# Optimization experiments

Measured on AMD Instinct MI355X. Metric: run time of the kernel, lower is better.

The kernel has to match this reference:

```python
import jax, jax.numpy as jnp
import numpy as np

B, N = 32, 512
IN, HID, HEADS, OUT = 128, 32, 4, 128
NEG_SLOPE = 0.2


def _ln(x, g, b, eps=1e-5):
    mu = x.mean(-1, keepdims=True)
    var = ((x - mu) ** 2).mean(-1, keepdims=True)
    return (x - mu) * jax.lax.rsqrt(var + eps) * g + b


def _gat(x, adj_mask, W, a_src, a_dst, average):
    # x: [B,N,F], adj_mask: [B,1,N,N] bool, W: [F,H,D], a_*: [H,D]
    h = jnp.einsum('bnf,fhd->bnhd', x, W)                      # [B,N,H,D]
    e_src = jnp.einsum('bnhd,hd->bhn', h, a_src)               # [B,H,N]
    e_dst = jnp.einsum('bnhd,hd->bhn', h, a_dst)
    e = jax.nn.leaky_relu(e_src[:, :, :, None] + e_dst[:, :, None, :], NEG_SLOPE)  # [B,H,N,N]
    e = jnp.where(adj_mask, e, jnp.asarray(-1e9, e.dtype))
    att = jax.nn.softmax(e, axis=-1)                           # masked softmax over neighbors
    out = jnp.einsum('bhnm,bmhd->bnhd', att, h)                # aggregate neighbor features
    if average:
        return out.mean(axis=2)                                # [B,N,D]
    return out.reshape(out.shape[0], out.shape[1], -1)         # concat heads [B,N,H*D]


def setup_inputs() -> dict:
    key = jax.random.key(0)
    ks = jax.random.split(key, 16)
    def nrm(k, shape, scale=0.05):
        return jax.random.normal(k, shape, dtype=jnp.float32) * scale
    return {
        'x': jax.random.normal(ks[0], (B, N, IN), dtype=jnp.float32),
        'graph': jax.random.randint(ks[1], (B, N, N), 0, 2, dtype=jnp.int32),
        'W0': nrm(ks[2], (IN, HEADS, HID)),
        'a_src0': nrm(ks[3], (HEADS, HID)),
        'a_dst0': nrm(ks[4], (HEADS, HID)),
        'W1': nrm(ks[5], (HEADS * HID, 1, OUT)),
        'a_src1': nrm(ks[6], (1, OUT)),
        'a_dst1': nrm(ks[7], (1, OUT)),
        'ln1_g': jnp.ones((IN + OUT,), jnp.float32), 'ln1_b': jnp.zeros((IN + OUT,), jnp.float32),
        'lin_W': nrm(ks[8], (IN + OUT, OUT)), 'lin_b': jnp.zeros((OUT,), jnp.float32),
        'me_W0': nrm(ks[9], (OUT, OUT)), 'me_b0': jnp.zeros((OUT,), jnp.float32),
        'me_W1': nrm(ks[10], (OUT, OUT)), 'me_b1': jnp.zeros((OUT,), jnp.float32),
        'ln2_g': jnp.ones((OUT,), jnp.float32), 'ln2_b': jnp.zeros((OUT,), jnp.float32),
        'oh_W': nrm(ks[11], (OUT, OUT)), 'oh_b': jnp.zeros((OUT,), jnp.float32),
        'ln3_g': jnp.ones((OUT,), jnp.float32), 'ln3_b': jnp.zeros((OUT,), jnp.float32),
    }


def reference(x, graph, W0, a_src0, a_dst0, W1, a_src1, a_dst1,
              ln1_g, ln1_b, lin_W, lin_b, me_W0, me_b0, me_W1, me_b1,
              ln2_g, ln2_b, oh_W, oh_b, ln3_g, ln3_b):
    eye = jnp.eye(N, dtype=bool)
    adj_mask = ((graph > 0) | eye)[:, None, :, :]              # self-loops, [B,1,N,N]
    m = _gat(x, adj_mask, W0, a_src0, a_dst0, average=False)   # [B,N,HEADS*HID]
    m = jax.nn.elu(m)
    m = _gat(m, adj_mask, W1, a_src1, a_dst1, average=True)    # [B,N,OUT]
    m = _ln(jnp.concatenate([x, m], axis=-1), ln1_g, ln1_b)    # ln1
    m = m @ lin_W + lin_b                                      # linear
    enc = jax.nn.gelu(m @ me_W0 + me_b0, approximate=False) @ me_W1 + me_b1
    out = _ln(m + enc, ln2_g, ln2_b)                           # ln2(residual)
    out = jax.nn.gelu(out @ oh_W + oh_b, approximate=False)
    out = _ln(out, ln3_g, ln3_b)                               # LN inside output_head
    return out
```

## Files before the change

### kernel.cpp

```cpp
#include <hip/hip_runtime.h>
#include <cmath>


typedef unsigned short ushort_t;
typedef __attribute__((ext_vector_type(8))) short short8;
typedef __attribute__((ext_vector_type(4))) float f32x4;

__device__ __forceinline__ float gelu_f(float v) {
    return 0.5f * v * (1.0f + erff(v * 0.70710678118654752f));
}
__device__ __forceinline__ ushort_t f2bf(float x) {
    union { float f; unsigned u; } v; v.f = x;
    return (ushort_t)((v.u + 0x7FFFu + ((v.u >> 16) & 1u)) >> 16);
}
__device__ __forceinline__ ushort_t f2bf_t(float x) {
    union { float f; unsigned u; } v; v.f = x;
    return (ushort_t)(v.u >> 16);
}

__global__ __launch_bounds__(256) void prep_wt(const float* __restrict__ lin_W,
        const float* __restrict__ me_W0, const float* __restrict__ me_W1,
        const float* __restrict__ oh_W, const float* __restrict__ W0,
        const float* __restrict__ W1, ushort_t* __restrict__ WT) {
    int i = blockIdx.x * 256 + threadIdx.x;
    if (i < 32768)       { int c = i >> 8, k = i & 255;                   WT[i] = f2bf(lin_W[k * 128 + c]); }
    else if (i < 49152)  { int j = i - 32768;  int c = j >> 7, k = j & 127; WT[i] = f2bf(me_W0[k * 128 + c]); }
    else if (i < 65536)  { int j = i - 49152;  int c = j >> 7, k = j & 127; WT[i] = f2bf(me_W1[k * 128 + c]); }
    else if (i < 81920)  { int j = i - 65536;  int c = j >> 7, k = j & 127; WT[i] = f2bf(oh_W[k * 128 + c]); }
    else if (i < 98304)  { int j = i - 81920;  int c = j >> 7, k = j & 127; WT[i] = f2bf(W0[k * 128 + c]); }
    else if (i < 114688) { int j = i - 98304;  int c = j >> 7, k = j & 127; WT[i] = f2bf(W1[k * 128 + c]); }
}

__global__ __launch_bounds__(256) void gemm_mfma0(const float* __restrict__ X,
        const ushort_t* __restrict__ WTr, ushort_t* __restrict__ Ht,
        const float* __restrict__ a_s, const float* __restrict__ a_d,
        float* __restrict__ es, float* __restrict__ ed) {
    __shared__ __align__(16) ushort_t abuf[16 * 128];
    __shared__ __align__(16) ushort_t tb[128 * 24];
    __shared__ float2 ered[8 * 16];
    const int tid = threadIdx.x;
    const int row0 = blockIdx.x * 16;
    const int b = row0 >> 9, m0 = row0 & 511;
    const int w = tid >> 6, lane = tid & 63;
    const int quad = lane >> 4, lid = lane & 15;
    {
        int r = tid >> 4, g = tid & 15;
        const float4* src = (const float4*)(X + (row0 + r) * 128 + g * 8);
        float4 a = src[0], bb = src[1];
        short8 p;
        p[0] = (short)f2bf(a.x);  p[1] = (short)f2bf(a.y);
        p[2] = (short)f2bf(a.z);  p[3] = (short)f2bf(a.w);
        p[4] = (short)f2bf(bb.x); p[5] = (short)f2bf(bb.y);
        p[6] = (short)f2bf(bb.z); p[7] = (short)f2bf(bb.w);
        *(short8*)&abuf[r * 128 + ((g ^ (r & 7)) * 8)] = p;
    }
    __syncthreads();
    short8 af[4];
#pragma unroll
    for (int kc = 0; kc < 4; kc++)
        af[kc] = *(const short8*)&abuf[lid * 128 + (((kc * 4 + quad) ^ (lid & 7)) * 8)];
    f32x4 C[2];
#pragma unroll
    for (int i = 0; i < 2; i++) {
        int ct = w + 4 * i;
        const ushort_t* bp = WTr + (ct * 16 + lid) * 128 + quad * 8;
        C[i] = (f32x4){0.f, 0.f, 0.f, 0.f};
#pragma unroll
        for (int kc = 0; kc < 4; kc++) {
            short8 bf = *(const short8*)&bp[kc * 32];
            C[i] = __builtin_amdgcn_mfma_f32_16x16x32_bf16(af[kc], bf, C[i], 0, 0, 0);
        }
    }
#pragma unroll
    for (int i = 0; i < 2; i++) {
        int ct = w + 4 * i, col = ct * 16 + lid;
        float as_c = a_s[col], ad_c = a_d[col];
        float s0[4], d0[4];
#pragma unroll
        for (int r = 0; r < 4; r++) { s0[r] = C[i][r] * as_c; d0[r] = C[i][r] * ad_c; }
#pragma unroll
        for (int st = 1; st <= 8; st <<= 1)
#pragma unroll
            for (int r = 0; r < 4; r++) {
                s0[r] += __shfl_xor(s0[r], st);
                d0[r] += __shfl_xor(d0[r], st);
            }
        if (lid == 0) {
#pragma unroll
            for (int r = 0; r < 4; r++)
                ered[ct * 16 + quad * 4 + r] = make_float2(s0[r], d0[r]);
        }
#pragma unroll
        for (int r = 0; r < 4; r++)
            tb[col * 24 + quad * 4 + r] = f2bf(C[i][r]);
    }
    __syncthreads();
    if (tid < 64) {
        int row = tid & 15, h = tid >> 4;
        float2 pa = ered[(2 * h) * 16 + row], pb = ered[(2 * h + 1) * 16 + row];
        es[(b * 4 + h) * 512 + m0 + row] = pa.x + pb.x;
        ed[(b * 4 + h) * 512 + m0 + row] = pa.y + pb.y;
    }
    {
        int c = tid >> 1, half = tid & 1;
        *(short8*)&Ht[b * 65536 + c * 512 + m0 + half * 8] = *(const short8*)&tb[c * 24 + half * 8];
    }
}

__global__ __launch_bounds__(256) void gat0_gemm(const ushort_t* __restrict__ Ht0,
        const float* __restrict__ es0, const float* __restrict__ ed0,
        const int* __restrict__ graph, const ushort_t* __restrict__ W1T,
        const float* __restrict__ a_s, const float* __restrict__ a_d,
        ushort_t* __restrict__ Ht1, float* __restrict__ es1, float* __restrict__ ed1) {
    __shared__ __align__(16) char smem[33024];
    ushort_t* hsb  = (ushort_t*)smem;
    ushort_t* ps   = (ushort_t*)(smem + 16384);
    float*    eds  = (float*)(smem + 24576);
    float*    ess  = (float*)(smem + 32768);
    ushort_t* abuf = (ushort_t*)(smem + 16384);
    ushort_t* tb   = (ushort_t*)(smem + 24576);
    float2*   ered = (float2*)(smem + 30720);
    const int tid = threadIdx.x;
    const int b = blockIdx.y, n0 = blockIdx.x * 16;
    const int lane = tid & 63, wv = tid >> 6;
    const int quad = lane >> 4, lid = lane & 15;
    const int pn = tid >> 4, pg = (tid >> 1) & 7, ph = tid & 1;
    for (int i = tid; i < 2048; i += 256) eds[i] = ed0[b * 2048 + i];
    if (tid < 64) ess[tid] = es0[b * 2048 + (tid >> 4) * 512 + n0 + (tid & 15)];
    const short8 onesf = {0x3F80, 0x3F80, 0x3F80, 0x3F80, 0x3F80, 0x3F80, 0x3F80, 0x3F80};
    f32x4 acc[2], dsf;
    acc[0] = (f32x4){0.f, 0.f, 0.f, 0.f};
    acc[1] = (f32x4){0.f, 0.f, 0.f, 0.f};
    dsf = (f32x4){0.f, 0.f, 0.f, 0.f};
    for (int mc = 0; mc < 512; mc += 64) {
        __syncthreads();
        {
            const ushort_t* src = Ht0 + b * 65536 + mc;
            for (int u = tid; u < 1024; u += 256) {
                int c = u >> 3, g = u & 7;
                *(short8*)&hsb[c * 64 + ((g ^ (c & 7)) * 8)] = *(const short8*)&src[c * 512 + g * 8];
            }
        }
        {
            int ng = n0 + pn, mbase = mc + pg * 8;
            const int* grow = graph + (b * 512 + ng) * 512 + mbase;
            int4 ga = *(const int4*)grow;
            int4 gb = *(const int4*)(grow + 4);
            int gv[8] = {ga.x, ga.y, ga.z, ga.w, gb.x, gb.y, gb.z, gb.w};
            bool keep[8];
#pragma unroll
            for (int j = 0; j < 8; j++)
                keep[j] = (gv[j] > 0) | ((mbase + j) == ng);
#pragma unroll
            for (int hi = 0; hi < 2; hi++) {
                int hh = ph * 2 + hi;
                float es_v = ess[hh * 16 + pn];
                float4 e0v = *(const float4*)&eds[hh * 512 + mbase];
                float4 e1v = *(const float4*)&eds[hh * 512 + mbase + 4];
                float ev[8] = {e0v.x, e0v.y, e0v.z, e0v.w, e1v.x, e1v.y, e1v.z, e1v.w};
                short8 pk;
#pragma unroll
                for (int j = 0; j < 8; j++) {
                    float e = es_v + ev[j];
                    e = fmaxf(e, 0.2f * e);
                    e = keep[j] ? e : -1e30f;
                    pk[j] = (short)f2bf_t(__expf(e));
                }
                int prow = hh * 16 + pn;
                *(short8*)&ps[prow * 64 + ((pg ^ (prow & 7)) * 8)] = pk;
            }
        }
        __syncthreads();
#pragma unroll
        for (int kc = 0; kc < 2; kc++) {
            const int gsw = ((kc * 4 + quad) ^ (lid & 7)) * 8;
            short8 a = *(const short8*)&ps[(wv * 16 + lid) * 64 + gsw];
            short8 b0f = *(const short8*)&hsb[(wv * 32 + lid) * 64 + gsw];
            short8 b1f = *(const short8*)&hsb[(wv * 32 + 16 + lid) * 64 + gsw];
            acc[0] = __builtin_amdgcn_mfma_f32_16x16x32_bf16(a, b0f, acc[0], 0, 0, 0);
            acc[1] = __builtin_amdgcn_mfma_f32_16x16x32_bf16(a, b1f, acc[1], 0, 0, 0);
            dsf = __builtin_amdgcn_mfma_f32_16x16x32_bf16(a, onesf, dsf, 0, 0, 0);
        }
    }
    __syncthreads();
#pragma unroll
    for (int reg = 0; reg < 4; reg++) {
        float inv = 1.0f / dsf[reg];
        int rw = quad * 4 + reg;
#pragma unroll
        for (int ch = 0; ch < 2; ch++) {
            float v = acc[ch][reg] * inv;
            v = v > 0.f ? v : expm1f(v);
            int col = wv * 32 + ch * 16 + lid;
            abuf[rw * 128 + (((col >> 3) ^ (rw & 7)) * 8) + (col & 7)] = f2bf(v);
        }
    }
    __syncthreads();
    short8 af[4];
#pragma unroll
    for (int kc = 0; kc < 4; kc++)
        af[kc] = *(const short8*)&abuf[lid * 128 + (((kc * 4 + quad) ^ (lid & 7)) * 8)];
    f32x4 C[2];
#pragma unroll
    for (int i = 0; i < 2; i++) {
        int ct = wv + 4 * i;
        const ushort_t* bp = W1T + (ct * 16 + lid) * 128 + quad * 8;
        C[i] = (f32x4){0.f, 0.f, 0.f, 0.f};
#pragma unroll
        for (int kc = 0; kc < 4; kc++) {
            short8 bf = *(const short8*)&bp[kc * 32];
            C[i] = __builtin_amdgcn_mfma_f32_16x16x32_bf16(af[kc], bf, C[i], 0, 0, 0);
        }
    }
#pragma unroll
    for (int i = 0; i < 2; i++) {
        int ct = wv + 4 * i, col = ct * 16 + lid;
        float as_c = a_s[col], ad_c = a_d[col];
        float s0[4], d0[4];
#pragma unroll
        for (int r = 0; r < 4; r++) { s0[r] = C[i][r] * as_c; d0[r] = C[i][r] * ad_c; }
#pragma unroll
        for (int st = 1; st <= 8; st <<= 1)
#pragma unroll
            for (int r = 0; r < 4; r++) {
                s0[r] += __shfl_xor(s0[r], st);
                d0[r] += __shfl_xor(d0[r], st);
            }
        if (lid == 0) {
#pragma unroll
            for (int r = 0; r < 4; r++)
                ered[ct * 16 + quad * 4 + r] = make_float2(s0[r], d0[r]);
        }
#pragma unroll
        for (int r = 0; r < 4; r++)
            tb[col * 24 + quad * 4 + r] = f2bf(C[i][r]);
    }
    __syncthreads();
    if (tid < 16) {
        float S = 0.f, D = 0.f;
#pragma unroll
        for (int ct = 0; ct < 8; ct++) { float2 p = ered[ct * 16 + tid]; S += p.x; D += p.y; }
        es1[b * 512 + n0 + tid] = S;
        ed1[b * 512 + n0 + tid] = D;
    }
    {
        int c = tid >> 1, half = tid & 1;
        *(short8*)&Ht1[b * 65536 + c * 512 + n0 + half * 8] = *(const short8*)&tb[c * 24 + half * 8];
    }
}

__global__ __launch_bounds__(256) void gat1_head(const ushort_t* __restrict__ Ht,
        const float* __restrict__ es1, const float* __restrict__ ed1,
        const int* __restrict__ graph, const float* __restrict__ x,
        const float* __restrict__ g1, const float* __restrict__ b1,
        const ushort_t* __restrict__ linT, const float* __restrict__ LB,
        const ushort_t* __restrict__ meT0, const float* __restrict__ B0,
        const ushort_t* __restrict__ meT1, const float* __restrict__ B1,
        const float* __restrict__ g2, const float* __restrict__ b2,
        const ushort_t* __restrict__ ohT, const float* __restrict__ ob,
        const float* __restrict__ g3, const float* __restrict__ b3,
        float* __restrict__ out) {
    __shared__ __align__(16) char smem[25472];
    ushort_t* hsb  = (ushort_t*)smem;
    ushort_t* ps   = (ushort_t*)(smem + 16384);
    float*    eds  = (float*)(smem + 18432);
    float*    ess  = (float*)(smem + 20480);
    ushort_t* ybuf = (ushort_t*)smem;
    ushort_t* abuf = (ushort_t*)(smem + 8192);
    ushort_t* tbuf = (ushort_t*)(smem + 12288);
    float*    gbuf = (float*)(smem + 16384);
    float2*   red  = (float2*)(smem + 24832);
    float2*   mvs  = (float2*)(smem + 25344);
    const int tid = threadIdx.x;
    const int b = blockIdx.y, n0 = blockIdx.x * 16;
    const int lane = tid & 63, wv = tid >> 6;
    const int quad = lane >> 4, lid = lane & 15;
    for (int i = tid; i < 512; i += 256) eds[i] = ed1[b * 512 + i];
    if (tid < 16) ess[tid] = es1[b * 512 + n0 + tid];
    const short8 onesf = {0x3F80, 0x3F80, 0x3F80, 0x3F80, 0x3F80, 0x3F80, 0x3F80, 0x3F80};
    f32x4 acc[2], dsf;
    acc[0] = (f32x4){0.f, 0.f, 0.f, 0.f};
    acc[1] = (f32x4){0.f, 0.f, 0.f, 0.f};
    dsf = (f32x4){0.f, 0.f, 0.f, 0.f};
    for (int mc = 0; mc < 512; mc += 64) {
        __syncthreads();
        {
            const ushort_t* src = Ht + b * 65536 + mc;
            for (int u = tid; u < 1024; u += 256) {
                int c = u >> 3, g = u & 7;
                *(short8*)&hsb[c * 64 + ((g ^ (c & 7)) * 8)] = *(const short8*)&src[c * 512 + g * 8];
            }
        }
        if (tid < 128) {
            int pn = tid >> 3, pg = tid & 7;
            int ng = n0 + pn, mbase = mc + pg * 8;
            const int* grow = graph + (b * 512 + ng) * 512 + mbase;
            int4 ga = *(const int4*)grow;
            int4 gb = *(const int4*)(grow + 4);
            int gv[8] = {ga.x, ga.y, ga.z, ga.w, gb.x, gb.y, gb.z, gb.w};
            float4 e0v = *(const float4*)&eds[mbase & 511];
            float4 e1v = *(const float4*)&eds[(mbase & 511) + 4];
            float ev[8] = {e0v.x, e0v.y, e0v.z, e0v.w, e1v.x, e1v.y, e1v.z, e1v.w};
            float es_v = ess[pn];
            short8 pk;
#pragma unroll
            for (int j = 0; j < 8; j++) {
                float e = es_v + ev[j];
                e = fmaxf(e, 0.2f * e);
                e = ((gv[j] > 0) | ((mbase + j) == ng)) ? e : -1e30f;
                pk[j] = (short)f2bf_t(__expf(e));
            }
            *(short8*)&ps[pn * 64 + ((pg ^ (pn & 7)) * 8)] = pk;
        }
        __syncthreads();
#pragma unroll
        for (int kc = 0; kc < 2; kc++) {
            const int gsw = ((kc * 4 + quad) ^ (lid & 7)) * 8;
            short8 a = *(const short8*)&ps[lid * 64 + gsw];
            short8 b0f = *(const short8*)&hsb[(wv * 32 + lid) * 64 + gsw];
            short8 b1f = *(const short8*)&hsb[(wv * 32 + 16 + lid) * 64 + gsw];
            acc[0] = __builtin_amdgcn_mfma_f32_16x16x32_bf16(a, b0f, acc[0], 0, 0, 0);
            acc[1] = __builtin_amdgcn_mfma_f32_16x16x32_bf16(a, b1f, acc[1], 0, 0, 0);
            dsf = __builtin_amdgcn_mfma_f32_16x16x32_bf16(a, onesf, dsf, 0, 0, 0);
        }
    }
    __syncthreads();
#pragma unroll
    for (int reg = 0; reg < 4; reg++) {
        float inv = 1.0f / dsf[reg];
        int rw = quad * 4 + reg;
#pragma unroll
        for (int ch = 0; ch < 2; ch++)
            gbuf[rw * 132 + wv * 32 + ch * 16 + lid] = acc[ch][reg] * inv;
    }
    __syncthreads();
    const int r = tid >> 4, c16 = tid & 15;
    const float4* xp = (const float4*)(x + (b * 512 + n0 + r) * 128);
    float4 vv4[4];
    float s = 0.f, ss = 0.f;
#pragma unroll
    for (int i = 0; i < 4; i++) {
        int c4 = c16 * 4 + i;
        float4 v = (c4 < 32) ? xp[c4] : *(const float4*)&gbuf[r * 132 + (c4 - 32) * 4];
        vv4[i] = v;
        s += v.x + v.y + v.z + v.w;
        ss += v.x * v.x + v.y * v.y + v.z * v.z + v.w * v.w;
    }
#pragma unroll
    for (int st = 1; st <= 8; st <<= 1) { s += __shfl_xor(s, st); ss += __shfl_xor(ss, st); }
    if (c16 == 0) {
        float mu = s * (1.f / 256.f);
        float var = ss * (1.f / 256.f) - mu * mu;
        mvs[r] = make_float2(mu, rsqrtf(var + 1e-5f));
    }
    __syncthreads();
    {
        float mu = mvs[r].x, rstd = mvs[r].y;
#pragma unroll
        for (int half = 0; half < 2; half++) {
            int g = c16 * 2 + half, c0 = g * 8;
            float va[8] = {vv4[half * 2].x, vv4[half * 2].y, vv4[half * 2].z, vv4[half * 2].w,
                           vv4[half * 2 + 1].x, vv4[half * 2 + 1].y, vv4[half * 2 + 1].z, vv4[half * 2 + 1].w};
            short8 p;
#pragma unroll
            for (int e = 0; e < 8; e++)
                p[e] = (short)f2bf((va[e] - mu) * rstd * g1[c0 + e] + b1[c0 + e]);
            *(short8*)&ybuf[r * 256 + ((g ^ (r & 7)) * 8)] = p;
        }
    }
    __syncthreads();
    short8 af8[8];
#pragma unroll
    for (int ks = 0; ks < 8; ks++)
        af8[ks] = *(const short8*)&ybuf[lid * 256 + (((ks * 4 + quad) ^ (lid & 7)) * 8)];
    f32x4 M2[2];
#pragma unroll
    for (int i = 0; i < 2; i++) {
        int ct = wv + 4 * i;
        const ushort_t* bp = linT + (ct * 16 + lid) * 256 + quad * 8;
        M2[i] = (f32x4){0.f, 0.f, 0.f, 0.f};
#pragma unroll
        for (int ks = 0; ks < 8; ks++) {
            short8 bf = *(const short8*)&bp[ks * 32];
            M2[i] = __builtin_amdgcn_mfma_f32_16x16x32_bf16(af8[ks], bf, M2[i], 0, 0, 0);
        }
        float bias = LB[ct * 16 + lid];
#pragma unroll
        for (int reg = 0; reg < 4; reg++) M2[i][reg] += bias;
        int col = ct * 16 + lid, g = col >> 3, pos = col & 7;
#pragma unroll
        for (int reg = 0; reg < 4; reg++) {
            int rw = quad * 4 + reg;
            abuf[rw * 128 + ((g ^ (rw & 7)) * 8) + pos] = f2bf(M2[i][reg]);
        }
    }
    __syncthreads();
    short8 at[4];
#pragma unroll
    for (int kc = 0; kc < 4; kc++)
        at[kc] = *(const short8*)&abuf[lid * 128 + (((kc * 4 + quad) ^ (lid & 7)) * 8)];
#pragma unroll
    for (int i = 0; i < 2; i++) {
        int ct = wv + 4 * i;
        const ushort_t* bp = meT0 + (ct * 16 + lid) * 128 + quad * 8;
        f32x4 C = (f32x4){0.f, 0.f, 0.f, 0.f};
#pragma unroll
        for (int kc = 0; kc < 4; kc++) {
            short8 bf = *(const short8*)&bp[kc * 32];
            C = __builtin_amdgcn_mfma_f32_16x16x32_bf16(at[kc], bf, C, 0, 0, 0);
        }
        int col = ct * 16 + lid, g = col >> 3, pos = col & 7;
        float bias = B0[col];
#pragma unroll
        for (int reg = 0; reg < 4; reg++) {
            int rw = quad * 4 + reg;
            tbuf[rw * 128 + ((g ^ (rw & 7)) * 8) + pos] = f2bf(gelu_f(C[reg] + bias));
        }
    }
    __syncthreads();
#pragma unroll
    for (int kc = 0; kc < 4; kc++)
        at[kc] = *(const short8*)&tbuf[lid * 128 + (((kc * 4 + quad) ^ (lid & 7)) * 8)];
    f32x4 R[2];
    float sr[4] = {0.f, 0.f, 0.f, 0.f}, ssr[4] = {0.f, 0.f, 0.f, 0.f};
#pragma unroll
    for (int i = 0; i < 2; i++) {
        int ct = wv + 4 * i;
        const ushort_t* bp = meT1 + (ct * 16 + lid) * 128 + quad * 8;
        f32x4 C = (f32x4){0.f, 0.f, 0.f, 0.f};
#pragma unroll
        for (int kc = 0; kc < 4; kc++) {
            short8 bf = *(const short8*)&bp[kc * 32];
            C = __builtin_amdgcn_mfma_f32_16x16x32_bf16(at[kc], bf, C, 0, 0, 0);
        }
        float bias = B1[ct * 16 + lid];
#pragma unroll
        for (int reg = 0; reg < 4; reg++) {
            float v = M2[i][reg] + C[reg] + bias;
            R[i][reg] = v;
            sr[reg] += v; ssr[reg] += v * v;
        }
    }
#pragma unroll
    for (int st = 1; st <= 8; st <<= 1)
#pragma unroll
        for (int reg = 0; reg < 4; reg++) {
            sr[reg] += __shfl_xor(sr[reg], st);
            ssr[reg] += __shfl_xor(ssr[reg], st);
        }
    if (lid == 0) {
#pragma unroll
        for (int reg = 0; reg < 4; reg++)
            red[wv * 16 + quad * 4 + reg] = make_float2(sr[reg], ssr[reg]);
    }
    __syncthreads();
    float mu2[4], rstd2[4];
#pragma unroll
    for (int reg = 0; reg < 4; reg++) {
        float S = 0.f, SS = 0.f;
#pragma unroll
        for (int w4 = 0; w4 < 4; w4++) {
            float2 p = red[w4 * 16 + quad * 4 + reg];
            S += p.x; SS += p.y;
        }
        mu2[reg] = S * (1.f / 128.f);
        float var = SS * (1.f / 128.f) - mu2[reg] * mu2[reg];
        rstd2[reg] = rsqrtf(var + 1e-5f);
    }
#pragma unroll
    for (int i = 0; i < 2; i++) {
        int col = (wv + 4 * i) * 16 + lid, g = col >> 3, pos = col & 7;
        float gv = g2[col], bv = b2[col];
#pragma unroll
        for (int reg = 0; reg < 4; reg++) {
            int rw = quad * 4 + reg;
            float v = (R[i][reg] - mu2[reg]) * rstd2[reg] * gv + bv;
            tbuf[rw * 128 + ((g ^ (rw & 7)) * 8) + pos] = f2bf(v);
        }
    }
    __syncthreads();
#pragma unroll
    for (int kc = 0; kc < 4; kc++)
        at[kc] = *(const short8*)&tbuf[lid * 128 + (((kc * 4 + quad) ^ (lid & 7)) * 8)];
    f32x4 V[2];
#pragma unroll
    for (int reg = 0; reg < 4; reg++) { sr[reg] = 0.f; ssr[reg] = 0.f; }
#pragma unroll
    for (int i = 0; i < 2; i++) {
        int ct = wv + 4 * i;
        const ushort_t* bp = ohT + (ct * 16 + lid) * 128 + quad * 8;
        f32x4 C = (f32x4){0.f, 0.f, 0.f, 0.f};
#pragma unroll
        for (int kc = 0; kc < 4; kc++) {
            short8 bf = *(const short8*)&bp[kc * 32];
            C = __builtin_amdgcn_mfma_f32_16x16x32_bf16(at[kc], bf, C, 0, 0, 0);
        }
        float bias = ob[ct * 16 + lid];
#pragma unroll
        for (int reg = 0; reg < 4; reg++) {
            float v = gelu_f(C[reg] + bias);
            V[i][reg] = v;
            sr[reg] += v; ssr[reg] += v * v;
        }
    }
#pragma unroll
    for (int st = 1; st <= 8; st <<= 1)
#pragma unroll
        for (int reg = 0; reg < 4; reg++) {
            sr[reg] += __shfl_xor(sr[reg], st);
            ssr[reg] += __shfl_xor(ssr[reg], st);
        }
    if (lid == 0) {
#pragma unroll
        for (int reg = 0; reg < 4; reg++)
            red[wv * 16 + quad * 4 + reg] = make_float2(sr[reg], ssr[reg]);
    }
    __syncthreads();
#pragma unroll
    for (int reg = 0; reg < 4; reg++) {
        float S = 0.f, SS = 0.f;
#pragma unroll
        for (int w4 = 0; w4 < 4; w4++) {
            float2 p = red[w4 * 16 + quad * 4 + reg];
            S += p.x; SS += p.y;
        }
        mu2[reg] = S * (1.f / 128.f);
        float var = SS * (1.f / 128.f) - mu2[reg] * mu2[reg];
        rstd2[reg] = rsqrtf(var + 1e-5f);
    }
#pragma unroll
    for (int i = 0; i < 2; i++) {
        int col = (wv + 4 * i) * 16 + lid;
        float gv = g3[col], bv = b3[col];
#pragma unroll
        for (int reg = 0; reg < 4; reg++)
            out[(b * 512 + n0 + quad * 4 + reg) * 128 + col] =
                (V[i][reg] - mu2[reg]) * rstd2[reg] * gv + bv;
    }
}

extern "C" void kernel_launch(void* const* d_in, const int* in_sizes, int n_in,
                              void* d_out, int out_size, void* d_ws, size_t ws_size,
                              hipStream_t stream) {
    const float* x      = (const float*)d_in[0];
    const int*   graph  = (const int*)d_in[1];
    const float* a_src0 = (const float*)d_in[3];
    const float* a_dst0 = (const float*)d_in[4];
    const float* a_src1 = (const float*)d_in[6];
    const float* a_dst1 = (const float*)d_in[7];
    float* out = (float*)d_out;

    float* ws  = (float*)d_ws;
    ushort_t* Ht0  = (ushort_t*)ws;
    ushort_t* Ht1  = Ht0 + 2097152;
    float*    e0s  = ws + 2097152;
    float*    e0d  = e0s + 65536;
    float*    e1s  = e0d + 65536;
    float*    e1d  = e1s + 16384;
    ushort_t* WT   = (ushort_t*)(e1d + 16384);
    ushort_t* linT = WT;
    ushort_t* meT0 = WT + 32768;
    ushort_t* meT1 = WT + 49152;
    ushort_t* ohT  = WT + 65536;
    ushort_t* W0T  = WT + 81920;
    ushort_t* W1T  = WT + 98304;

    prep_wt<<<448, 256, 0, stream>>>((const float*)d_in[10], (const float*)d_in[12],
                                     (const float*)d_in[14], (const float*)d_in[18],
                                     (const float*)d_in[2], (const float*)d_in[5], WT);
    gemm_mfma0<<<1024, 256, 0, stream>>>(x, W0T, Ht0, a_src0, a_dst0, e0s, e0d);
    gat0_gemm<<<dim3(32, 32), 256, 0, stream>>>(Ht0, e0s, e0d, graph, W1T,
                                                a_src1, a_dst1, Ht1, e1s, e1d);
    gat1_head<<<dim3(32, 32), 256, 0, stream>>>(Ht1, e1s, e1d, graph, x,
                                                (const float*)d_in[8], (const float*)d_in[9],
                                                linT, (const float*)d_in[11],
                                                meT0, (const float*)d_in[13],
                                                meT1, (const float*)d_in[15],
                                                (const float*)d_in[16], (const float*)d_in[17],
                                                ohT, (const float*)d_in[19],
                                                (const float*)d_in[20], (const float*)d_in[21],
                                                out);
}
```

Measured before the change: 198.5 us.

## Load GAT operands directly into MFMA registers instead of staging via LDS

```diff
diff --git a/kernel.cpp b/kernel.cpp
--- a/kernel.cpp
+++ b/kernel.cpp
@@ -35,34 +35,29 @@
         const ushort_t* __restrict__ WTr, ushort_t* __restrict__ Ht,
         const float* __restrict__ a_s, const float* __restrict__ a_d,
         float* __restrict__ es, float* __restrict__ ed) {
-    __shared__ __align__(16) ushort_t abuf[16 * 128];
     __shared__ __align__(16) ushort_t tb[128 * 24];
-    __shared__ float2 ered[8 * 16];
     const int tid = threadIdx.x;
     const int row0 = blockIdx.x * 16;
     const int b = row0 >> 9, m0 = row0 & 511;
-    const int w = tid >> 6, lane = tid & 63;
+    const int wv = tid >> 6, lane = tid & 63;
     const int quad = lane >> 4, lid = lane & 15;
-    {
-        int r = tid >> 4, g = tid & 15;
-        const float4* src = (const float4*)(X + (row0 + r) * 128 + g * 8);
-        float4 a = src[0], bb = src[1];
+    short8 af[4];
+#pragma unroll
+    for (int kc = 0; kc < 4; kc++) {
+        const float4* xp = (const float4*)(X + (row0 + lid) * 128 + kc * 32 + quad * 8);
+        float4 a = xp[0], bb = xp[1];
         short8 p;
         p[0] = (short)f2bf(a.x);  p[1] = (short)f2bf(a.y);
         p[2] = (short)f2bf(a.z);  p[3] = (short)f2bf(a.w);
         p[4] = (short)f2bf(bb.x); p[5] = (short)f2bf(bb.y);
         p[6] = (short)f2bf(bb.z); p[7] = (short)f2bf(bb.w);
-        *(short8*)&abuf[r * 128 + ((g ^ (r & 7)) * 8)] = p;
-    }
-    __syncthreads();
-    short8 af[4];
-#pragma unroll
-    for (int kc = 0; kc < 4; kc++)
-        af[kc] = *(const short8*)&abuf[lid * 128 + (((kc * 4 + quad) ^ (lid & 7)) * 8)];
+        af[kc] = p;
+    }
     f32x4 C[2];
-#pragma unroll
-    for (int i = 0; i < 2; i++) {
-        int ct = w + 4 * i;
+    float s0[4] = {0.f, 0.f, 0.f, 0.f}, d0[4] = {0.f, 0.f, 0.f, 0.f};
+#pragma unroll
+    for (int i = 0; i < 2; i++) {
+        int ct = 2 * wv + i;
         const ushort_t* bp = WTr + (ct * 16 + lid) * 128 + quad * 8;
         C[i] = (f32x4){0.f, 0.f, 0.f, 0.f};
 #pragma unroll
@@ -70,37 +65,33 @@
             short8 bf = *(const short8*)&bp[kc * 32];
             C[i] = __builtin_amdgcn_mfma_f32_16x16x32_bf16(af[kc], bf, C[i], 0, 0, 0);
         }
-    }
-#pragma unroll
-    for (int i = 0; i < 2; i++) {
-        int ct = w + 4 * i, col = ct * 16 + lid;
+        int col = ct * 16 + lid;
         float as_c = a_s[col], ad_c = a_d[col];
-        float s0[4], d0[4];
-#pragma unroll
-        for (int r = 0; r < 4; r++) { s0[r] = C[i][r] * as_c; d0[r] = C[i][r] * ad_c; }
-#pragma unroll
-        for (int st = 1; st <= 8; st <<= 1)
-#pragma unroll
-            for (int r = 0; r < 4; r++) {
-                s0[r] += __shfl_xor(s0[r], st);
-                d0[r] += __shfl_xor(d0[r], st);
-            }
-        if (lid == 0) {
-#pragma unroll
-            for (int r = 0; r < 4; r++)
-                ered[ct * 16 + quad * 4 + r] = make_float2(s0[r], d0[r]);
+#pragma unroll
+        for (int r = 0; r < 4; r++) {
+            s0[r] = fmaf(C[i][r], as_c, s0[r]);
+            d0[r] = fmaf(C[i][r], ad_c, d0[r]);
         }
 #pragma unroll
         for (int r = 0; r < 4; r++)
             tb[col * 24 + quad * 4 + r] = f2bf(C[i][r]);
     }
-    __syncthreads();
-    if (tid < 64) {
-        int row = tid & 15, h = tid >> 4;
-        float2 pa = ered[(2 * h) * 16 + row], pb = ered[(2 * h + 1) * 16 + row];
-        es[(b * 4 + h) * 512 + m0 + row] = pa.x + pb.x;
-        ed[(b * 4 + h) * 512 + m0 + row] = pa.y + pb.y;
-    }
+#pragma unroll
+    for (int st = 1; st <= 8; st <<= 1)
+#pragma unroll
+        for (int r = 0; r < 4; r++) {
+            s0[r] += __shfl_xor(s0[r], st);
+            d0[r] += __shfl_xor(d0[r], st);
+        }
+    if (lid == 0) {
+#pragma unroll
+        for (int r = 0; r < 4; r++) {
+            int n = m0 + quad * 4 + r;
+            es[(b * 4 + wv) * 512 + n] = s0[r];
+            ed[(b * 4 + wv) * 512 + n] = d0[r];
+        }
+    }
+    __syncthreads();
     {
         int c = tid >> 1, half = tid & 1;
         *(short8*)&Ht[b * 65536 + c * 512 + m0 + half * 8] = *(const short8*)&tb[c * 24 + half * 8];
@@ -112,77 +103,47 @@
         const int* __restrict__ graph, const ushort_t* __restrict__ W1T,
         const float* __restrict__ a_s, const float* __restrict__ a_d,
         ushort_t* __restrict__ Ht1, float* __restrict__ es1, float* __restrict__ ed1) {
-    __shared__ __align__(16) char smem[33024];
-    ushort_t* hsb  = (ushort_t*)smem;
-    ushort_t* ps   = (ushort_t*)(smem + 16384);
-    float*    eds  = (float*)(smem + 24576);
-    float*    ess  = (float*)(smem + 32768);
-    ushort_t* abuf = (ushort_t*)(smem + 16384);
-    ushort_t* tb   = (ushort_t*)(smem + 24576);
-    float2*   ered = (float2*)(smem + 30720);
+    __shared__ __align__(16) ushort_t abuf[16 * 128];
+    __shared__ __align__(16) ushort_t tb[128 * 24];
+    __shared__ float2 ered[8 * 16];
     const int tid = threadIdx.x;
     const int b = blockIdx.y, n0 = blockIdx.x * 16;
-    const int lane = tid & 63, wv = tid >> 6;
+    const int wv = tid >> 6, lane = tid & 63;
     const int quad = lane >> 4, lid = lane & 15;
-    const int pn = tid >> 4, pg = (tid >> 1) & 7, ph = tid & 1;
-    for (int i = tid; i < 2048; i += 256) eds[i] = ed0[b * 2048 + i];
-    if (tid < 64) ess[tid] = es0[b * 2048 + (tid >> 4) * 512 + n0 + (tid & 15)];
+    const int n_mine = n0 + lid;
+    const int* gptr = graph + (b * 512 + n_mine) * 512 + quad * 8;
+    const float* edp = ed0 + (b * 4 + wv) * 512 + quad * 8;
+    const float es_v = es0[(b * 4 + wv) * 512 + n_mine];
+    const ushort_t* hb0 = Ht0 + b * 65536 + (wv * 32 + lid) * 512;
+    const ushort_t* hb1 = hb0 + 16 * 512;
     const short8 onesf = {0x3F80, 0x3F80, 0x3F80, 0x3F80, 0x3F80, 0x3F80, 0x3F80, 0x3F80};
     f32x4 acc[2], dsf;
     acc[0] = (f32x4){0.f, 0.f, 0.f, 0.f};
     acc[1] = (f32x4){0.f, 0.f, 0.f, 0.f};
     dsf = (f32x4){0.f, 0.f, 0.f, 0.f};
-    for (int mc = 0; mc < 512; mc += 64) {
-        __syncthreads();
-        {
-            const ushort_t* src = Ht0 + b * 65536 + mc;
-            for (int u = tid; u < 1024; u += 256) {
-                int c = u >> 3, g = u & 7;
-                *(short8*)&hsb[c * 64 + ((g ^ (c & 7)) * 8)] = *(const short8*)&src[c * 512 + g * 8];
-            }
-        }
-        {
-            int ng = n0 + pn, mbase = mc + pg * 8;
-            const int* grow = graph + (b * 512 + ng) * 512 + mbase;
-            int4 ga = *(const int4*)grow;
-            int4 gb = *(const int4*)(grow + 4);
-            int gv[8] = {ga.x, ga.y, ga.z, ga.w, gb.x, gb.y, gb.z, gb.w};
-            bool keep[8];
-#pragma unroll
-            for (int j = 0; j < 8; j++)
-                keep[j] = (gv[j] > 0) | ((mbase + j) == ng);
-#pragma unroll
-            for (int hi = 0; hi < 2; hi++) {
-                int hh = ph * 2 + hi;
-                float es_v = ess[hh * 16 + pn];
-                float4 e0v = *(const float4*)&eds[hh * 512 + mbase];
-                float4 e1v = *(const float4*)&eds[hh * 512 + mbase + 4];
-                float ev[8] = {e0v.x, e0v.y, e0v.z, e0v.w, e1v.x, e1v.y, e1v.z, e1v.w};
-                short8 pk;
-#pragma unroll
-                for (int j = 0; j < 8; j++) {
-                    float e = es_v + ev[j];
-                    e = fmaxf(e, 0.2f * e);
-                    e = keep[j] ? e : -1e30f;
-                    pk[j] = (short)f2bf_t(__expf(e));
-                }
-                int prow = hh * 16 + pn;
-                *(short8*)&ps[prow * 64 + ((pg ^ (prow & 7)) * 8)] = pk;
-            }
-        }
-        __syncthreads();
-#pragma unroll
-        for (int kc = 0; kc < 2; kc++) {
-            const int gsw = ((kc * 4 + quad) ^ (lid & 7)) * 8;
-            short8 a = *(const short8*)&ps[(wv * 16 + lid) * 64 + gsw];
-            short8 b0f = *(const short8*)&hsb[(wv * 32 + lid) * 64 + gsw];
-            short8 b1f = *(const short8*)&hsb[(wv * 32 + 16 + lid) * 64 + gsw];
-            acc[0] = __builtin_amdgcn_mfma_f32_16x16x32_bf16(a, b0f, acc[0], 0, 0, 0);
-            acc[1] = __builtin_amdgcn_mfma_f32_16x16x32_bf16(a, b1f, acc[1], 0, 0, 0);
-            dsf = __builtin_amdgcn_mfma_f32_16x16x32_bf16(a, onesf, dsf, 0, 0, 0);
-        }
-    }
-    __syncthreads();
+#pragma unroll 4
+    for (int mcc = 0; mcc < 16; mcc++) {
+        const int mbase = mcc * 32 + quad * 8;
+        int4 ga = *(const int4*)(gptr + mcc * 32);
+        int4 gb = *(const int4*)(gptr + mcc * 32 + 4);
+        float4 e0v = *(const float4*)(edp + mcc * 32);
+        float4 e1v = *(const float4*)(edp + mcc * 32 + 4);
+        int gv[8] = {ga.x, ga.y, ga.z, ga.w, gb.x, gb.y, gb.z, gb.w};
+        float ev[8] = {e0v.x, e0v.y, e0v.z, e0v.w, e1v.x, e1v.y, e1v.z, e1v.w};
+        short8 pk;
+#pragma unroll
+        for (int j = 0; j < 8; j++) {
+            float e = es_v + ev[j];
+            e = fmaxf(e, 0.2f * e);
+            e = ((gv[j] > 0) | ((mbase + j) == n_mine)) ? e : -1e30f;
+            pk[j] = (short)f2bf_t(__expf(e));
+        }
+        short8 b0 = *(const short8*)&hb0[mbase];
+        short8 b1 = *(const short8*)&hb1[mbase];
+        acc[0] = __builtin_amdgcn_mfma_f32_16x16x32_bf16(pk, b0, acc[0], 0, 0, 0);
+        acc[1] = __builtin_amdgcn_mfma_f32_16x16x32_bf16(pk, b1, acc[1], 0, 0, 0);
+        dsf = __builtin_amdgcn_mfma_f32_16x16x32_bf16(pk, onesf, dsf, 0, 0, 0);
+    }
 #pragma unroll
     for (int reg = 0; reg < 4; reg++) {
         float inv = 1.0f / dsf[reg];
@@ -260,71 +221,50 @@
         const ushort_t* __restrict__ ohT, const float* __restrict__ ob,
         const float* __restrict__ g3, const float* __restrict__ b3,
         float* __restrict__ out) {
-    __shared__ __align__(16) char smem[25472];
-    ushort_t* hsb  = (ushort_t*)smem;
-    ushort_t* ps   = (ushort_t*)(smem + 16384);
-    float*    eds  = (float*)(smem + 18432);
-    float*    ess  = (float*)(smem + 20480);
-    ushort_t* ybuf = (ushort_t*)smem;
-    ushort_t* abuf = (ushort_t*)(smem + 8192);
-    ushort_t* tbuf = (ushort_t*)(smem + 12288);
-    float*    gbuf = (float*)(smem + 16384);
-    float2*   red  = (float2*)(smem + 24832);
-    float2*   mvs  = (float2*)(smem + 25344);
+    __shared__ __align__(16) float    gbuf[16 * 132];
+    __shared__ __align__(16) ushort_t ybuf[16 * 256];
+    __shared__ __align__(16) ushort_t abuf[16 * 128];
+    __shared__ __align__(16) ushort_t tbuf[16 * 128];
+    __shared__ float2 red[4 * 16];
+    __shared__ float2 mvs[16];
     const int tid = threadIdx.x;
     const int b = blockIdx.y, n0 = blockIdx.x * 16;
-    const int lane = tid & 63, wv = tid >> 6;
+    const int wv = tid >> 6, lane = tid & 63;
     const int quad = lane >> 4, lid = lane & 15;
-    for (int i = tid; i < 512; i += 256) eds[i] = ed1[b * 512 + i];
-    if (tid < 16) ess[tid] = es1[b * 512 + n0 + tid];
+    const int n_mine = n0 + lid;
+    const int* gptr = graph + (b * 512 + n_mine) * 512 + quad * 8;
+    const float* edp = ed1 + b * 512 + quad * 8;
+    const float es_v = es1[b * 512 + n_mine];
+    const ushort_t* hb0 = Ht + b * 65536 + (wv * 32 + lid) * 512;
+    const ushort_t* hb1 = hb0 + 16 * 512;
     const short8 onesf = {0x3F80, 0x3F80, 0x3F80, 0x3F80, 0x3F80, 0x3F80, 0x3F80, 0x3F80};
     f32x4 acc[2], dsf;
     acc[0] = (f32x4){0.f, 0.f, 0.f, 0.f};
     acc[1] = (f32x4){0.f, 0.f, 0.f, 0.f};
     dsf = (f32x4){0.f, 0.f, 0.f, 0.f};
-    for (int mc = 0; mc < 512; mc += 64) {
-        __syncthreads();
-        {
-            const ushort_t* src = Ht + b * 65536 + mc;
-            for (int u = tid; u < 1024; u += 256) {
-                int c = u >> 3, g = u & 7;
-                *(short8*)&hsb[c * 64 + ((g ^ (c & 7)) * 8)] = *(const short8*)&src[c * 512 + g * 8];
-            }
-        }
-        if (tid < 128) {
-            int pn = tid >> 3, pg = tid & 7;
-            int ng = n0 + pn, mbase = mc + pg * 8;
-            const int* grow = graph + (b * 512 + ng) * 512 + mbase;
-            int4 ga = *(const int4*)grow;
-            int4 gb = *(const int4*)(grow + 4);
-            int gv[8] = {ga.x, ga.y, ga.z, ga.w, gb.x, gb.y, gb.z, gb.w};
-            float4 e0v = *(const float4*)&eds[mbase & 511];
-            float4 e1v = *(const float4*)&eds[(mbase & 511) + 4];
-            float ev[8] = {e0v.x, e0v.y, e0v.z, e0v.w, e1v.x, e1v.y, e1v.z, e1v.w};
-            float es_v = ess[pn];
-            short8 pk;
-#pragma unroll
-            for (int j = 0; j < 8; j++) {
-                float e = es_v + ev[j];
-                e = fmaxf(e, 0.2f * e);
-                e = ((gv[j] > 0) | ((mbase + j) == ng)) ? e : -1e30f;
-                pk[j] = (short)f2bf_t(__expf(e));
-            }
-            *(short8*)&ps[pn * 64 + ((pg ^ (pn & 7)) * 8)] = pk;
-        }
-        __syncthreads();
-#pragma unroll
-        for (int kc = 0; kc < 2; kc++) {
-            const int gsw = ((kc * 4 + quad) ^ (lid & 7)) * 8;
-            short8 a = *(const short8*)&ps[lid * 64 + gsw];
-            short8 b0f = *(const short8*)&hsb[(wv * 32 + lid) * 64 + gsw];
-            short8 b1f = *(const short8*)&hsb[(wv * 32 + 16 + lid) * 64 + gsw];
-            acc[0] = __builtin_amdgcn_mfma_f32_16x16x32_bf16(a, b0f, acc[0], 0, 0, 0);
-            acc[1] = __builtin_amdgcn_mfma_f32_16x16x32_bf16(a, b1f, acc[1], 0, 0, 0);
-            dsf = __builtin_amdgcn_mfma_f32_16x16x32_bf16(a, onesf, dsf, 0, 0, 0);
-        }
-    }
-    __syncthreads();
+#pragma unroll 4
+    for (int mcc = 0; mcc < 16; mcc++) {
+        const int mbase = mcc * 32 + quad * 8;
+        int4 ga = *(const int4*)(gptr + mcc * 32);
+        int4 gb = *(const int4*)(gptr + mcc * 32 + 4);
+        float4 e0v = *(const float4*)(edp + mcc * 32);
+        float4 e1v = *(const float4*)(edp + mcc * 32 + 4);
+        int gv[8] = {ga.x, ga.y, ga.z, ga.w, gb.x, gb.y, gb.z, gb.w};
+        float ev[8] = {e0v.x, e0v.y, e0v.z, e0v.w, e1v.x, e1v.y, e1v.z, e1v.w};
+        short8 pk;
+#pragma unroll
+        for (int j = 0; j < 8; j++) {
+            float e = es_v + ev[j];
+            e = fmaxf(e, 0.2f * e);
+            e = ((gv[j] > 0) | ((mbase + j) == n_mine)) ? e : -1e30f;
+            pk[j] = (short)f2bf_t(__expf(e));
+        }
+        short8 b0 = *(const short8*)&hb0[mbase];
+        short8 b1 = *(const short8*)&hb1[mbase];
+        acc[0] = __builtin_amdgcn_mfma_f32_16x16x32_bf16(pk, b0, acc[0], 0, 0, 0);
+        acc[1] = __builtin_amdgcn_mfma_f32_16x16x32_bf16(pk, b1, acc[1], 0, 0, 0);
+        dsf = __builtin_amdgcn_mfma_f32_16x16x32_bf16(pk, onesf, dsf, 0, 0, 0);
+    }
 #pragma unroll
     for (int reg = 0; reg < 4; reg++) {
         float inv = 1.0f / dsf[reg];
```

After: 225.2 us. +13.4%, slower.

## Compute attention weights in registers per wave and prefetch next chunk without block barriers

Applied to the files above, without the earlier changes.

```diff
diff --git a/kernel.cpp b/kernel.cpp
--- a/kernel.cpp
+++ b/kernel.cpp
@@ -112,74 +112,81 @@
         const int* __restrict__ graph, const ushort_t* __restrict__ W1T,
         const float* __restrict__ a_s, const float* __restrict__ a_d,
         ushort_t* __restrict__ Ht1, float* __restrict__ es1, float* __restrict__ ed1) {
-    __shared__ __align__(16) char smem[33024];
+    __shared__ __align__(16) char smem[32768];
     ushort_t* hsb  = (ushort_t*)smem;
-    ushort_t* ps   = (ushort_t*)(smem + 16384);
-    float*    eds  = (float*)(smem + 24576);
-    float*    ess  = (float*)(smem + 32768);
-    ushort_t* abuf = (ushort_t*)(smem + 16384);
-    ushort_t* tb   = (ushort_t*)(smem + 24576);
-    float2*   ered = (float2*)(smem + 30720);
+    ushort_t* abuf = (ushort_t*)smem;
+    ushort_t* tb   = (ushort_t*)(smem + 4096);
+    float2*   ered = (float2*)(smem + 10240);
     const int tid = threadIdx.x;
     const int b = blockIdx.y, n0 = blockIdx.x * 16;
-    const int lane = tid & 63, wv = tid >> 6;
+    const int wv = tid >> 6, lane = tid & 63;
     const int quad = lane >> 4, lid = lane & 15;
-    const int pn = tid >> 4, pg = (tid >> 1) & 7, ph = tid & 1;
-    for (int i = tid; i < 2048; i += 256) eds[i] = ed0[b * 2048 + i];
-    if (tid < 64) ess[tid] = es0[b * 2048 + (tid >> 4) * 512 + n0 + (tid & 15)];
+    const int n_mine = n0 + lid;
+    const int sc = lane & 31, sg0 = (lane >> 5) * 4;
+    const ushort_t* sp = Ht0 + b * 65536 + (wv * 32 + sc) * 512 + sg0 * 8;
+    const int* gp = graph + (b * 512 + n_mine) * 512 + quad * 8;
+    const float* edp = ed0 + (b * 4 + wv) * 512 + quad * 8;
+    const float es_v = es0[(b * 4 + wv) * 512 + n_mine];
     const short8 onesf = {0x3F80, 0x3F80, 0x3F80, 0x3F80, 0x3F80, 0x3F80, 0x3F80, 0x3F80};
     f32x4 acc[2], dsf;
     acc[0] = (f32x4){0.f, 0.f, 0.f, 0.f};
     acc[1] = (f32x4){0.f, 0.f, 0.f, 0.f};
     dsf = (f32x4){0.f, 0.f, 0.f, 0.f};
-    for (int mc = 0; mc < 512; mc += 64) {
-        __syncthreads();
-        {
-            const ushort_t* src = Ht0 + b * 65536 + mc;
-            for (int u = tid; u < 1024; u += 256) {
-                int c = u >> 3, g = u & 7;
-                *(short8*)&hsb[c * 64 + ((g ^ (c & 7)) * 8)] = *(const short8*)&src[c * 512 + g * 8];
+    short8 stg[4];
+    int4 gr[4];
+    float4 er[4];
+#pragma unroll
+    for (int t = 0; t < 4; t++) stg[t] = *(const short8*)&sp[t * 8];
+#pragma unroll
+    for (int kc = 0; kc < 2; kc++) {
+        gr[kc * 2]     = *(const int4*)(gp + kc * 32);
+        gr[kc * 2 + 1] = *(const int4*)(gp + kc * 32 + 4);
+        er[kc * 2]     = *(const float4*)(edp + kc * 32);
+        er[kc * 2 + 1] = *(const float4*)(edp + kc * 32 + 4);
+    }
+#pragma unroll 2
+    for (int mcc = 0; mcc < 8; mcc++) {
+        ushort_t* wb = hsb + (mcc & 1) * 8192 + wv * 2048;
+#pragma unroll
+        for (int t = 0; t < 4; t++) {
+            int g = sg0 + t;
+            *(short8*)&wb[sc * 64 + ((g ^ (sc & 7)) * 8)] = stg[t];
+        }
+        short8 pk[2];
+#pragma unroll
+        for (int kc = 0; kc < 2; kc++) {
+            int mb = mcc * 64 + kc * 32 + quad * 8;
+            int gv[8] = {gr[kc * 2].x, gr[kc * 2].y, gr[kc * 2].z, gr[kc * 2].w,
+                         gr[kc * 2 + 1].x, gr[kc * 2 + 1].y, gr[kc * 2 + 1].z, gr[kc * 2 + 1].w};
+            float ev[8] = {er[kc * 2].x, er[kc * 2].y, er[kc * 2].z, er[kc * 2].w,
+                           er[kc * 2 + 1].x, er[kc * 2 + 1].y, er[kc * 2 + 1].z, er[kc * 2 + 1].w};
+#pragma unroll
+            for (int j = 0; j < 8; j++) {
+                float e = es_v + ev[j];
+                e = fmaxf(e, 0.2f * e);
+                e = ((gv[j] > 0) | ((mb + j) == n_mine)) ? e : -1e30f;
+                pk[kc][j] = (short)f2bf_t(__expf(e));
             }
         }
-        {
-            int ng = n0 + pn, mbase = mc + pg * 8;
-            const int* grow = graph + (b * 512 + ng) * 512 + mbase;
-            int4 ga = *(const int4*)grow;
-            int4 gb = *(const int4*)(grow + 4);
-            int gv[8] = {ga.x, ga.y, ga.z, ga.w, gb.x, gb.y, gb.z, gb.w};
-            bool keep[8];
-#pragma unroll
-            for (int j = 0; j < 8; j++)
-                keep[j] = (gv[j] > 0) | ((mbase + j) == ng);
-#pragma unroll
-            for (int hi = 0; hi < 2; hi++) {
-                int hh = ph * 2 + hi;
-                float es_v = ess[hh * 16 + pn];
-                float4 e0v = *(const float4*)&eds[hh * 512 + mbase];
-                float4 e1v = *(const float4*)&eds[hh * 512 + mbase + 4];
-                float ev[8] = {e0v.x, e0v.y, e0v.z, e0v.w, e1v.x, e1v.y, e1v.z, e1v.w};
-                short8 pk;
-#pragma unroll
-                for (int j = 0; j < 8; j++) {
-                    float e = es_v + ev[j];
-                    e = fmaxf(e, 0.2f * e);
-                    e = keep[j] ? e : -1e30f;
-                    pk[j] = (short)f2bf_t(__expf(e));
-                }
-                int prow = hh * 16 + pn;
-                *(short8*)&ps[prow * 64 + ((pg ^ (prow & 7)) * 8)] = pk;
+        if (mcc < 7) {
+#pragma unroll
+            for (int t = 0; t < 4; t++) stg[t] = *(const short8*)&sp[(mcc + 1) * 64 + t * 8];
+#pragma unroll
+            for (int kc = 0; kc < 2; kc++) {
+                gr[kc * 2]     = *(const int4*)(gp + (mcc + 1) * 64 + kc * 32);
+                gr[kc * 2 + 1] = *(const int4*)(gp + (mcc + 1) * 64 + kc * 32 + 4);
+                er[kc * 2]     = *(const float4*)(edp + (mcc + 1) * 64 + kc * 32);
+                er[kc * 2 + 1] = *(const float4*)(edp + (mcc + 1) * 64 + kc * 32 + 4);
             }
         }
-        __syncthreads();
 #pragma unroll
         for (int kc = 0; kc < 2; kc++) {
             const int gsw = ((kc * 4 + quad) ^ (lid & 7)) * 8;
-            short8 a = *(const short8*)&ps[(wv * 16 + lid) * 64 + gsw];
-            short8 b0f = *(const short8*)&hsb[(wv * 32 + lid) * 64 + gsw];
-            short8 b1f = *(const short8*)&hsb[(wv * 32 + 16 + lid) * 64 + gsw];
-            acc[0] = __builtin_amdgcn_mfma_f32_16x16x32_bf16(a, b0f, acc[0], 0, 0, 0);
-            acc[1] = __builtin_amdgcn_mfma_f32_16x16x32_bf16(a, b1f, acc[1], 0, 0, 0);
-            dsf = __builtin_amdgcn_mfma_f32_16x16x32_bf16(a, onesf, dsf, 0, 0, 0);
+            short8 b0 = *(const short8*)&wb[lid * 64 + gsw];
+            short8 b1 = *(const short8*)&wb[(16 + lid) * 64 + gsw];
+            acc[0] = __builtin_amdgcn_mfma_f32_16x16x32_bf16(pk[kc], b0, acc[0], 0, 0, 0);
+            acc[1] = __builtin_amdgcn_mfma_f32_16x16x32_bf16(pk[kc], b1, acc[1], 0, 0, 0);
+            dsf = __builtin_amdgcn_mfma_f32_16x16x32_bf16(pk[kc], onesf, dsf, 0, 0, 0);
         }
     }
     __syncthreads();
@@ -260,68 +267,84 @@
         const ushort_t* __restrict__ ohT, const float* __restrict__ ob,
         const float* __restrict__ g3, const float* __restrict__ b3,
         float* __restrict__ out) {
-    __shared__ __align__(16) char smem[25472];
+    __shared__ __align__(16) char smem[32768];
     ushort_t* hsb  = (ushort_t*)smem;
-    ushort_t* ps   = (ushort_t*)(smem + 16384);
-    float*    eds  = (float*)(smem + 18432);
-    float*    ess  = (float*)(smem + 20480);
-    ushort_t* ybuf = (ushort_t*)smem;
-    ushort_t* abuf = (ushort_t*)(smem + 8192);
-    ushort_t* tbuf = (ushort_t*)(smem + 12288);
-    float*    gbuf = (float*)(smem + 16384);
+    float*    gbuf = (float*)smem;
+    ushort_t* ybuf = (ushort_t*)(smem + 8448);
+    ushort_t* abuf = (ushort_t*)(smem + 16640);
+    ushort_t* tbuf = (ushort_t*)(smem + 20736);
     float2*   red  = (float2*)(smem + 24832);
     float2*   mvs  = (float2*)(smem + 25344);
     const int tid = threadIdx.x;
     const int b = blockIdx.y, n0 = blockIdx.x * 16;
-    const int lane = tid & 63, wv = tid >> 6;
+    const int wv = tid >> 6, lane = tid & 63;
     const int quad = lane >> 4, lid = lane & 15;
-    for (int i = tid; i < 512; i += 256) eds[i] = ed1[b * 512 + i];
-    if (tid < 16) ess[tid] = es1[b * 512 + n0 + tid];
+    const int n_mine = n0 + lid;
+    const int sc = lane & 31, sg0 = (lane >> 5) * 4;
+    const ushort_t* sp = Ht + b * 65536 + (wv * 32 + sc) * 512 + sg0 * 8;
+    const int* gp = graph + (b * 512 + n_mine) * 512 + quad * 8;
+    const float* edp = ed1 + b * 512 + quad * 8;
+    const float es_v = es1[b * 512 + n_mine];
     const short8 onesf = {0x3F80, 0x3F80, 0x3F80, 0x3F80, 0x3F80, 0x3F80, 0x3F80, 0x3F80};
     f32x4 acc[2], dsf;
     acc[0] = (f32x4){0.f, 0.f, 0.f, 0.f};
     acc[1] = (f32x4){0.f, 0.f, 0.f, 0.f};
     dsf = (f32x4){0.f, 0.f, 0.f, 0.f};
-    for (int mc = 0; mc < 512; mc += 64) {
-        __syncthreads();
-        {
-            const ushort_t* src = Ht + b * 65536 + mc;
-            for (int u = tid; u < 1024; u += 256) {
-                int c = u >> 3, g = u & 7;
-                *(short8*)&hsb[c * 64 + ((g ^ (c & 7)) * 8)] = *(const short8*)&src[c * 512 + g * 8];
-            }
-        }
-        if (tid < 128) {
-            int pn = tid >> 3, pg = tid & 7;
-            int ng = n0 + pn, mbase = mc + pg * 8;
-            const int* grow = graph + (b * 512 + ng) * 512 + mbase;
-            int4 ga = *(const int4*)grow;
-            int4 gb = *(const int4*)(grow + 4);
-            int gv[8] = {ga.x, ga.y, ga.z, ga.w, gb.x, gb.y, gb.z, gb.w};
-            float4 e0v = *(const float4*)&eds[mbase & 511];
-            float4 e1v = *(const float4*)&eds[(mbase & 511) + 4];
-            float ev[8] = {e0v.x, e0v.y, e0v.z, e0v.w, e1v.x, e1v.y, e1v.z, e1v.w};
-            float es_v = ess[pn];
-            short8 pk;
+    short8 stg[4];
+    int4 gr[4];
+    float4 er[4];
+#pragma unroll
+    for (int t = 0; t < 4; t++) stg[t] = *(const short8*)&sp[t * 8];
+#pragma unroll
+    for (int kc = 0; kc < 2; kc++) {
+        gr[kc * 2]     = *(const int4*)(gp + kc * 32);
+        gr[kc * 2 + 1] = *(const int4*)(gp + kc * 32 + 4);
+        er[kc * 2]     = *(const float4*)(edp + kc * 32);
+        er[kc * 2 + 1] = *(const float4*)(edp + kc * 32 + 4);
+    }
+#pragma unroll 2
+    for (int mcc = 0; mcc < 8; mcc++) {
+        ushort_t* wb = hsb + (mcc & 1) * 8192 + wv * 2048;
+#pragma unroll
+        for (int t = 0; t < 4; t++) {
+            int g = sg0 + t;
+            *(short8*)&wb[sc * 64 + ((g ^ (sc & 7)) * 8)] = stg[t];
+        }
+        short8 pk[2];
+#pragma unroll
+        for (int kc = 0; kc < 2; kc++) {
+            int mb = mcc * 64 + kc * 32 + quad * 8;
+            int gv[8] = {gr[kc * 2].x, gr[kc * 2].y, gr[kc * 2].z, gr[kc * 2].w,
+                         gr[kc * 2 + 1].x, gr[kc * 2 + 1].y, gr[kc * 2 + 1].z, gr[kc * 2 + 1].w};
+            float ev[8] = {er[kc * 2].x, er[kc * 2].y, er[kc * 2].z, er[kc * 2].w,
+                           er[kc * 2 + 1].x, er[kc * 2 + 1].y, er[kc * 2 + 1].z, er[kc * 2 + 1].w};
 #pragma unroll
             for (int j = 0; j < 8; j++) {
                 float e = es_v + ev[j];
                 e = fmaxf(e, 0.2f * e);
-                e = ((gv[j] > 0) | ((mbase + j) == ng)) ? e : -1e30f;
-                pk[j] = (short)f2bf_t(__expf(e));
+                e = ((gv[j] > 0) | ((mb + j) == n_mine)) ? e : -1e30f;
+                pk[kc][j] = (short)f2bf_t(__expf(e));
             }
-            *(short8*)&ps[pn * 64 + ((pg ^ (pn & 7)) * 8)] = pk;
-        }
-        __syncthreads();
+        }
+        if (mcc < 7) {
+#pragma unroll
+            for (int t = 0; t < 4; t++) stg[t] = *(const short8*)&sp[(mcc + 1) * 64 + t * 8];
+#pragma unroll
+            for (int kc = 0; kc < 2; kc++) {
+                gr[kc * 2]     = *(const int4*)(gp + (mcc + 1) * 64 + kc * 32);
+                gr[kc * 2 + 1] = *(const int4*)(gp + (mcc + 1) * 64 + kc * 32 + 4);
+                er[kc * 2]     = *(const float4*)(edp + (mcc + 1) * 64 + kc * 32);
+                er[kc * 2 + 1] = *(const float4*)(edp + (mcc + 1) * 64 + kc * 32 + 4);
+            }
+        }
 #pragma unroll
         for (int kc = 0; kc < 2; kc++) {
             const int gsw = ((kc * 4 + quad) ^ (lid & 7)) * 8;
-            short8 a = *(const short8*)&ps[lid * 64 + gsw];
-            short8 b0f = *(const short8*)&hsb[(wv * 32 + lid) * 64 + gsw];
-            short8 b1f = *(const short8*)&hsb[(wv * 32 + 16 + lid) * 64 + gsw];
-            acc[0] = __builtin_amdgcn_mfma_f32_16x16x32_bf16(a, b0f, acc[0], 0, 0, 0);
-            acc[1] = __builtin_amdgcn_mfma_f32_16x16x32_bf16(a, b1f, acc[1], 0, 0, 0);
-            dsf = __builtin_amdgcn_mfma_f32_16x16x32_bf16(a, onesf, dsf, 0, 0, 0);
+            short8 b0 = *(const short8*)&wb[lid * 64 + gsw];
+            short8 b1 = *(const short8*)&wb[(16 + lid) * 64 + gsw];
+            acc[0] = __builtin_amdgcn_mfma_f32_16x16x32_bf16(pk[kc], b0, acc[0], 0, 0, 0);
+            acc[1] = __builtin_amdgcn_mfma_f32_16x16x32_bf16(pk[kc], b1, acc[1], 0, 0, 0);
+            dsf = __builtin_amdgcn_mfma_f32_16x16x32_bf16(pk[kc], onesf, dsf, 0, 0, 0);
         }
     }
     __syncthreads();
```

Result: slower. 223.7 us (+12.7%).
